# Kernel optimization log

Hardware: AMD Instinct MI355X
Metric: run time of the kernel (lower is better)

The kernel has to match this reference:

```python
import jax, jax.numpy as jnp
import numpy as np

BN_EPS = 1e-5


def _bn_relu(h, gamma, beta):
    # BatchNorm1d in training mode: normalize over (batch, length) per channel
    mean = h.mean(axis=(0, 2), keepdims=True)
    var = h.var(axis=(0, 2), keepdims=True)
    h = (h - mean) * jax.lax.rsqrt(var + BN_EPS)
    h = h * gamma[None, :, None] + beta[None, :, None]
    return jax.nn.relu(h)


def _gather(ldesc, idx):
    # ldesc: [B, D, N], idx: [B, M] -> [B, D, M]
    B, D, N = ldesc.shape
    M = idx.shape[1]
    return jnp.take_along_axis(ldesc, jnp.broadcast_to(idx[:, None, :], (B, D, M)), axis=2)


def _scatter_mean(src, idx, N):
    # per-batch scatter-mean: src [B, D, M], idx [B, M] -> [B, D, N]
    def one(s, i):
        D = s.shape[0]
        sums = jnp.zeros((D, N), s.dtype).at[:, i].add(s)
        cnts = jnp.zeros((N,), s.dtype).at[i].add(1.0)
        return sums / jnp.maximum(cnts, 1.0)[None, :]
    return jax.vmap(one)(src, idx)


def _endpoint_update(ldesc, line_enc, idx, W1, b1, g1, bt1, W2, b2):
    B, D, _ = ldesc.shape
    ld = _gather(ldesc, idx)                                   # [B, D, 2L]
    # flip endpoint pairs: neighbor endpoint of each endpoint
    neigh = ld.reshape(B, D, -1, 2)[..., ::-1].reshape(B, D, -1)
    msg = jnp.concatenate([ld, neigh, line_enc], axis=1)       # [B, 3D, 2L]
    h = jnp.einsum('oc,bcm->bom', W1, msg) + b1[None, :, None]  # Conv1d k=1
    h = _bn_relu(h, g1, bt1)
    out = jnp.einsum('oc,bcm->bom', W2, h) + b2[None, :, None]
    return out                                                  # [B, D, 2L]


def setup_inputs() -> dict:
    key = jax.random.key(0)
    ks = jax.random.split(key, 12)
    B, D, N, M = 8, 256, 8192, 8192
    inp = {
        'ldesc0': jax.random.normal(ks[0], (B, D, N), jnp.float32),
        'ldesc1': jax.random.normal(ks[1], (B, D, N), jnp.float32),
        'line_enc0': jax.random.normal(ks[2], (B, D, M), jnp.float32),
        'line_enc1': jax.random.normal(ks[3], (B, D, M), jnp.float32),
        'lines_junc_idx0': jax.random.randint(ks[4], (B, M), 0, N),
        'lines_junc_idx1': jax.random.randint(ks[5], (B, M), 0, N),
        'W1': jax.random.normal(ks[6], (2 * D, 3 * D), jnp.float32) * (1.0 / np.sqrt(3 * D)),
        'b1': jnp.zeros((2 * D,), jnp.float32),
        'g1': jnp.ones((2 * D,), jnp.float32),
        'bt1': jnp.zeros((2 * D,), jnp.float32),
        'W2': jax.random.normal(ks[7], (D, 2 * D), jnp.float32) * (1.0 / np.sqrt(2 * D)),
        'b2': jnp.zeros((D,), jnp.float32),
    }
    return inp


def reference(ldesc0, ldesc1, line_enc0, line_enc1, lines_junc_idx0, lines_junc_idx1,
              W1, b1, g1, bt1, W2, b2):
    N = ldesc0.shape[2]
    up0 = _endpoint_update(ldesc0, line_enc0, lines_junc_idx0, W1, b1, g1, bt1, W2, b2)
    up1 = _endpoint_update(ldesc1, line_enc1, lines_junc_idx1, W1, b1, g1, bt1, W2, b2)
    out0 = ldesc0 + _scatter_mean(up0, lines_junc_idx0, N)
    out1 = ldesc1 + _scatter_mean(up1, lines_junc_idx1, N)
    return (out0, out1)
```

## Files before the change

### kernel.cpp

```cpp
#include <hip/hip_runtime.h>
#include <hip/hip_bf16.h>

#define B_  8
#define D_  256
#define N_  8192
#define M_  8192
#define O1_ 512
#define K1_ 768
#define K2_ 512

typedef unsigned short u16;
typedef __attribute__((ext_vector_type(8))) short bf8;
typedef __attribute__((ext_vector_type(4))) float f4;

static __device__ __forceinline__ float bf2f(u16 u) {
    unsigned v = ((unsigned)u) << 16;
    return __uint_as_float(v);
}
static __device__ __forceinline__ u16 f2bf(float f) {
    __hip_bfloat16 h = __float2bfloat16(f);
    return *reinterpret_cast<u16*>(&h);
}
static __device__ __forceinline__ void gl_lds16(const u16* g, u16* l) {
    __builtin_amdgcn_global_load_lds((const __attribute__((address_space(1))) void*)g,
                                     (__attribute__((address_space(3))) void*)l, 16, 0, 0);
}
static __device__ __forceinline__ int swz64(int r) {
    return (((r >> 1) & 1) << 4) | (((r >> 2) & 1) << 5);
}

__global__ __launch_bounds__(256) void k_transpose_all(const float* __restrict__ s0, const float* __restrict__ s1,
                                                       const float* __restrict__ s2, const float* __restrict__ s3,
                                                       u16* __restrict__ dA, u16* __restrict__ dB) {
    __shared__ float t[32][33];
    const int z = blockIdx.z;
    const int sel = z >> 3, b = z & 7;
    const float* src = (sel == 0) ? s0 : (sel == 1) ? s1 : (sel == 2) ? s2 : s3;
    u16* dst = ((sel < 2) ? dA : dB) + (size_t)(sel & 1) * B_ * N_ * D_;
    const int c0 = blockIdx.x * 32, r0 = blockIdx.y * 32;
    const int tx = threadIdx.x, ty = threadIdx.y;
    const float* s = src + (size_t)b * D_ * N_;
    u16* d = dst + (size_t)b * N_ * D_;
#pragma unroll
    for (int i = 0; i < 4; ++i) {
        int r = r0 + ty + i * 8;
        t[ty + i * 8][tx] = s[(size_t)r * N_ + (c0 + tx)];
    }
    __syncthreads();
#pragma unroll
    for (int i = 0; i < 4; ++i) {
        int c = c0 + ty + i * 8;
        d[(size_t)c * D_ + (r0 + tx)] = f2bf(t[tx][ty + i * 8]);
    }
}

__global__ __launch_bounds__(256) void k_convert_w(const float* __restrict__ W1, const float* __restrict__ W2,
                                                   u16* __restrict__ W1b, u16* __restrict__ W2b) {
    int i = blockIdx.x * 256 + threadIdx.x;
    const int n1 = O1_ * K1_;
    const int n2 = D_ * K2_;
    if (i < n1) W1b[i] = f2bf(W1[i]);
    int j = i - n1;
    if (j >= 0 && j < n2) W2b[j] = f2bf(W2[j]);
}

#define NT1 12
__global__ __launch_bounds__(512, 2) void k_gemm1(const u16* __restrict__ W1b,
                                                  const u16* __restrict__ Tld2,
                                                  const u16* __restrict__ Tle2,
                                                  const int* __restrict__ idx0,
                                                  const int* __restrict__ idx1,
                                                  u16* __restrict__ hbuf2) {
    __shared__ u16 LA[2][2][256][32];
    __shared__ u16 LB[2][2][256][32];
    const int z  = blockIdx.z;
    const int side = z >> 3, b = z & 7;
    const u16* Tld = Tld2 + (size_t)side * B_ * N_ * D_;
    const u16* Tle = Tle2 + (size_t)side * B_ * N_ * D_;
    const int* idx = side ? idx1 : idx0;
    u16* hbuf = hbuf2 + (size_t)side * B_ * M_ * O1_;
    const int o0 = blockIdx.y * 256;
    const int m0 = blockIdx.x * 256;
    const int tid = threadIdx.x;
    const int w = tid >> 6, l = tid & 63;
    const int wr = w >> 2;
    const int wc = w & 3;

    const int srow   = tid >> 2;
    const int schunk = (tid & 3) * 16;

    int na[2], nb[2], mm[2];
    const u16* aS[2];
    int bcolu[2];
#pragma unroll
    for (int j = 0; j < 2; ++j) {
        int r = j * 128 + srow;
        int m = m0 + r;
        mm[j] = m;
        na[j] = idx[b * M_ + m];
        nb[j] = idx[b * M_ + (m ^ 1)];
        int swu = (schunk ^ swz64(r)) >> 1;
        aS[j]   = W1b + (size_t)(o0 + r) * K1_ + swu;
        bcolu[j] = swu;
    }

    int aOff[8], bOff[4];
#pragma unroll
    for (int i = 0; i < 8; ++i) {
        int r = wr * 128 + i * 16 + (l & 15);
        aOff[i] = r * 32 + ((((l >> 4) * 16) ^ swz64(r)) >> 1);
    }
#pragma unroll
    for (int j = 0; j < 4; ++j) {
        int r = wc * 64 + j * 16 + (l & 15);
        bOff[j] = r * 32 + ((((l >> 4) * 16) ^ swz64(r)) >> 1);
    }

#define STAGE_A1(kt, ks, buf)                                                        \
    {                                                                                \
        _Pragma("unroll")                                                            \
        for (int j = 0; j < 2; ++j)                                                  \
            gl_lds16(aS[j] + (kt) * 64 + (ks) * 32, &LA[buf][ks][j * 128][0] + tid * 8); \
    }
#define STAGE_B1(kt, ks, buf)                                                        \
    {                                                                                \
        const int seg = (kt) >> 2;                                                   \
        const int cb  = ((kt) & 3) * 64 + (ks) * 32;                                 \
        _Pragma("unroll")                                                            \
        for (int j = 0; j < 2; ++j) {                                                \
            const u16* s;                                                            \
            if (seg == 0)      s = Tld + (size_t)(b * N_ + na[j]) * D_ + cb + bcolu[j]; \
            else if (seg == 1) s = Tld + (size_t)(b * N_ + nb[j]) * D_ + cb + bcolu[j]; \
            else               s = Tle + (size_t)(b * M_ + mm[j]) * D_ + cb + bcolu[j]; \
            gl_lds16(s, &LB[buf][ks][j * 128][0] + tid * 8);                         \
        }                                                                            \
    }

    f4 acc[8][4];
#pragma unroll
    for (int i = 0; i < 8; ++i)
#pragma unroll
        for (int j = 0; j < 4; ++j) acc[i][j] = {0.f, 0.f, 0.f, 0.f};

    STAGE_A1(0, 0, 0); STAGE_B1(0, 0, 0);
    STAGE_A1(0, 1, 0); STAGE_B1(0, 1, 0);
    STAGE_A1(1, 0, 1); STAGE_B1(1, 0, 1);
    asm volatile("s_waitcnt vmcnt(8)" ::: "memory");
    __builtin_amdgcn_s_barrier();
    __builtin_amdgcn_sched_barrier(0);

    for (int t = 0; t < NT1; ++t) {
        const int bufp = t & 1, nbuf = bufp ^ 1;
        const u16* baseA0 = &LA[bufp][0][0][0];
        const u16* baseA1 = &LA[bufp][1][0][0];
        const u16* baseB0 = &LB[bufp][0][0][0];
        const u16* baseB1 = &LB[bufp][1][0][0];
        bf8 aF[4], bF[4];

#pragma unroll
        for (int j = 0; j < 4; ++j) bF[j] = *reinterpret_cast<const bf8*>(baseB0 + bOff[j]);
#pragma unroll
        for (int ii = 0; ii < 4; ++ii) aF[ii] = *reinterpret_cast<const bf8*>(baseA0 + aOff[ii]);
        if (t + 1 < NT1) STAGE_A1(t + 1, 1, nbuf);
        __builtin_amdgcn_s_barrier();
        asm volatile("s_waitcnt lgkmcnt(0)" ::: "memory");
        __builtin_amdgcn_sched_barrier(0);
        __builtin_amdgcn_s_setprio(1);
#pragma unroll
        for (int ii = 0; ii < 4; ++ii)
#pragma unroll
            for (int j = 0; j < 4; ++j)
                acc[ii][j] = __builtin_amdgcn_mfma_f32_16x16x32_bf16(aF[ii], bF[j], acc[ii][j], 0, 0, 0);
        __builtin_amdgcn_s_setprio(0);
        __builtin_amdgcn_s_barrier();
        __builtin_amdgcn_sched_barrier(0);

#pragma unroll
        for (int ii = 0; ii < 4; ++ii) aF[ii] = *reinterpret_cast<const bf8*>(baseA0 + aOff[4 + ii]);
        if (t + 1 < NT1) STAGE_B1(t + 1, 1, nbuf);
        __builtin_amdgcn_s_barrier();
        asm volatile("s_waitcnt lgkmcnt(0)" ::: "memory");
        __builtin_amdgcn_sched_barrier(0);
        __builtin_amdgcn_s_setprio(1);
#pragma unroll
        for (int ii = 0; ii < 4; ++ii)
#pragma unroll
            for (int j = 0; j < 4; ++j)
                acc[4 + ii][j] = __builtin_amdgcn_mfma_f32_16x16x32_bf16(aF[ii], bF[j], acc[4 + ii][j], 0, 0, 0);
        __builtin_amdgcn_s_setprio(0);
        if (t < NT1 - 2) asm volatile("s_waitcnt vmcnt(8)" ::: "memory");
        else             asm volatile("s_waitcnt vmcnt(0)" ::: "memory");
        __builtin_amdgcn_s_barrier();
        __builtin_amdgcn_sched_barrier(0);

#pragma unroll
        for (int j = 0; j < 4; ++j) bF[j] = *reinterpret_cast<const bf8*>(baseB1 + bOff[j]);
#pragma unroll
        for (int ii = 0; ii < 4; ++ii) aF[ii] = *reinterpret_cast<const bf8*>(baseA1 + aOff[ii]);
        if (t + 2 < NT1) STAGE_A1(t + 2, 0, bufp);
        __builtin_amdgcn_s_barrier();
        asm volatile("s_waitcnt lgkmcnt(0)" ::: "memory");
        __builtin_amdgcn_sched_barrier(0);
        __builtin_amdgcn_s_setprio(1);
#pragma unroll
        for (int ii = 0; ii < 4; ++ii)
#pragma unroll
            for (int j = 0; j < 4; ++j)
                acc[ii][j] = __builtin_amdgcn_mfma_f32_16x16x32_bf16(aF[ii], bF[j], acc[ii][j], 0, 0, 0);
        __builtin_amdgcn_s_setprio(0);
        __builtin_amdgcn_s_barrier();
        __builtin_amdgcn_sched_barrier(0);

#pragma unroll
        for (int ii = 0; ii < 4; ++ii) aF[ii] = *reinterpret_cast<const bf8*>(baseA1 + aOff[4 + ii]);
        if (t + 2 < NT1) STAGE_B1(t + 2, 0, bufp);
        __builtin_amdgcn_s_barrier();
        asm volatile("s_waitcnt lgkmcnt(0)" ::: "memory");
        __builtin_amdgcn_sched_barrier(0);
        __builtin_amdgcn_s_setprio(1);
#pragma unroll
        for (int ii = 0; ii < 4; ++ii)
#pragma unroll
            for (int j = 0; j < 4; ++j)
                acc[4 + ii][j] = __builtin_amdgcn_mfma_f32_16x16x32_bf16(aF[ii], bF[j], acc[4 + ii][j], 0, 0, 0);
        __builtin_amdgcn_s_setprio(0);
        if (t < NT1 - 2) asm volatile("s_waitcnt vmcnt(8)" ::: "memory");
        else             asm volatile("s_waitcnt vmcnt(0)" ::: "memory");
        __builtin_amdgcn_s_barrier();
        __builtin_amdgcn_sched_barrier(0);
    }
#undef STAGE_A1
#undef STAGE_B1

#pragma unroll
    for (int j = 0; j < 4; ++j) {
        int m = m0 + wc * 64 + j * 16 + (l & 15);
        size_t rowbase = (size_t)(b * M_ + m) * O1_;
#pragma unroll
        for (int i = 0; i < 8; ++i) {
            int orow = o0 + wr * 128 + i * 16 + (l >> 4) * 4;
            ushort4 pk;
            pk.x = f2bf(acc[i][j].x);
            pk.y = f2bf(acc[i][j].y);
            pk.z = f2bf(acc[i][j].z);
            pk.w = f2bf(acc[i][j].w);
            *reinterpret_cast<ushort4*>(&hbuf[rowbase + orow]) = pk;
        }
    }
}

__global__ __launch_bounds__(256) void k_stats(const u16* __restrict__ hbuf2, float* __restrict__ stats) {
    const int side = blockIdx.x >> 8;
    const int blk  = blockIdx.x & 255;
    const u16* hb = hbuf2 + (size_t)side * B_ * M_ * O1_;
    float* st = stats + side * 1024;
    const int t = threadIdx.x;
    const size_t row0 = (size_t)blk * 256;
    float s0 = 0.f, q0 = 0.f, s1 = 0.f, q1 = 0.f;
    for (int r = 0; r < 256; ++r) {
        const u16* p = hb + (row0 + r) * O1_;
        float v0 = bf2f(p[t]);
        float v1 = bf2f(p[t + 256]);
        s0 += v0; q0 += v0 * v0;
        s1 += v1; q1 += v1 * v1;
    }
    atomicAdd(&st[t], s0);
    atomicAdd(&st[O1_ + t], q0);
    atomicAdd(&st[t + 256], s1);
    atomicAdd(&st[O1_ + t + 256], q1);
}

__global__ void k_finalize_ac(const float* __restrict__ stats, const float* __restrict__ g1,
                              const float* __restrict__ bt1, float* __restrict__ ac) {
    int i = blockIdx.x * 256 + threadIdx.x;
    if (i >= 1024) return;
    int side = i >> 9, o = i & 511;
    const float* st = stats + side * 1024;
    const float inv = 1.0f / ((float)B_ * (float)M_);
    float mean = st[o] * inv;
    float var  = st[O1_ + o] * inv - mean * mean;
    var = fmaxf(var, 0.0f);
    float a = g1[o] * rsqrtf(var + 1e-5f);
    ac[side * 1024 + o] = a;
    ac[side * 1024 + O1_ + o] = bt1[o] - mean * a;
}

__global__ void k_count_int(const int* __restrict__ idx0, const int* __restrict__ idx1, int* __restrict__ cnt2) {
    int i = blockIdx.x * 256 + threadIdx.x;
    if (i < 2 * B_ * M_) {
        int side = i >> 16, j = i & 65535;
        const int* idx = side ? idx1 : idx0;
        atomicAdd(&cnt2[side * B_ * N_ + (j >> 13) * N_ + idx[j]], 1);
    }
}

__global__ __launch_bounds__(1024) void k_scan(const int* __restrict__ cnt2, int* __restrict__ offs2,
                                               int* __restrict__ fill2) {
    __shared__ int wsum[1024];
    const int base = blockIdx.x * N_;
    const int t = threadIdx.x;
    int v[8]; int s = 0;
#pragma unroll
    for (int k = 0; k < 8; ++k) { v[k] = cnt2[base + t * 8 + k]; s += v[k]; }
    wsum[t] = s;
    __syncthreads();
    for (int off = 1; off < 1024; off <<= 1) {
        int add = (t >= off) ? wsum[t - off] : 0;
        __syncthreads();
        wsum[t] += add;
        __syncthreads();
    }
    int run = (t > 0) ? wsum[t - 1] : 0;
#pragma unroll
    for (int k = 0; k < 8; ++k) {
        offs2[base + t * 8 + k] = run;
        fill2[base + t * 8 + k] = run;
        run += v[k];
    }
}

__global__ void k_fill(const int* __restrict__ idx0, const int* __restrict__ idx1,
                       int* __restrict__ fill2, int* __restrict__ mlist2) {
    int i = blockIdx.x * 256 + threadIdx.x;
    if (i < 2 * B_ * M_) {
        int side = i >> 16, j = i & 65535;
        const int* idx = side ? idx1 : idx0;
        int b = j >> 13, m = j & (M_ - 1);
        int pos = atomicAdd(&fill2[side * B_ * N_ + b * N_ + idx[j]], 1);
        mlist2[(size_t)side * B_ * M_ + b * M_ + pos] = m;
    }
}

__global__ __launch_bounds__(256) void k_gemm2(const u16* __restrict__ W2b,
                                               const u16* __restrict__ hbuf2,
                                               const float* __restrict__ ac,
                                               const float* __restrict__ b2,
                                               u16* __restrict__ up2) {
    __shared__ u16 At[128 * 32];
    __shared__ u16 Bt[128 * 32];
    __shared__ float acs[1024];
    const int z = blockIdx.z;
    const int side = z >> 3, b = z & 7;
    const u16* hbuf = hbuf2 + (size_t)side * B_ * M_ * O1_;
    u16* up = up2 + (size_t)side * B_ * M_ * D_;
    const float* acp = ac + side * 1024;
    const int d0 = blockIdx.y * 128;
    const int m0 = blockIdx.x * 128;
    const int tid = threadIdx.x;
    const int w = tid >> 6, l = tid & 63;
    const int lr = l >> 2, lc = (l & 3) * 8;

    acs[tid]       = acp[tid];
    acs[tid + 256] = acp[tid + 256];
    acs[tid + 512] = acp[tid + 512];
    acs[tid + 768] = acp[tid + 768];

    const u16* pA[2]; const u16* pB[2];
#pragma unroll
    for (int t = 0; t < 2; ++t) {
        int row = t * 64 + w * 16 + lr;
        pA[t] = W2b + (size_t)(d0 + row) * K2_ + lc;
        int m  = m0 + row;
        pB[t] = hbuf + (size_t)(b * M_ + m) * O1_ + lc;
    }
    const int wr = w >> 1, wc = w & 1;
    f4 acc[4][4];
#pragma unroll
    for (int i = 0; i < 4; ++i)
#pragma unroll
        for (int j = 0; j < 4; ++j) acc[i][j] = {0.f, 0.f, 0.f, 0.f};

    const int aoff = (wr * 64 + (l & 15)) * 32 + (l >> 4) * 8;
    const int boff = (wc * 64 + (l & 15)) * 32 + (l >> 4) * 8;
    const int bdst = (w * 16 + lr) * 32 + lc;

    __syncthreads();

    for (int kk = 0; kk < 16; ++kk) {
        const int o = kk * 32 + lc;
        f4 A0 = *reinterpret_cast<const f4*>(&acs[o]);
        f4 A1 = *reinterpret_cast<const f4*>(&acs[o + 4]);
        f4 C0 = *reinterpret_cast<const f4*>(&acs[512 + o]);
        f4 C1 = *reinterpret_cast<const f4*>(&acs[512 + o + 4]);
#pragma unroll
        for (int t = 0; t < 2; ++t) {
            gl_lds16(pA[t] + kk * 32, At + (t * 64 + w * 16) * 32);
            const ushort4* ps = reinterpret_cast<const ushort4*>(pB[t] + kk * 32);
            ushort4 v0 = ps[0], v1 = ps[1];
            union { ushort4 u4[2]; bf8 v8; } pk;
            pk.u4[0].x = f2bf(fmaxf(bf2f(v0.x) * A0.x + C0.x, 0.0f));
            pk.u4[0].y = f2bf(fmaxf(bf2f(v0.y) * A0.y + C0.y, 0.0f));
            pk.u4[0].z = f2bf(fmaxf(bf2f(v0.z) * A0.z + C0.z, 0.0f));
            pk.u4[0].w = f2bf(fmaxf(bf2f(v0.w) * A0.w + C0.w, 0.0f));
            pk.u4[1].x = f2bf(fmaxf(bf2f(v1.x) * A1.x + C1.x, 0.0f));
            pk.u4[1].y = f2bf(fmaxf(bf2f(v1.y) * A1.y + C1.y, 0.0f));
            pk.u4[1].z = f2bf(fmaxf(bf2f(v1.z) * A1.z + C1.z, 0.0f));
            pk.u4[1].w = f2bf(fmaxf(bf2f(v1.w) * A1.w + C1.w, 0.0f));
            *reinterpret_cast<bf8*>(&Bt[t * 64 * 32 + bdst]) = pk.v8;
        }
        __syncthreads();
        bf8 aF[4], bF[4];
#pragma unroll
        for (int i = 0; i < 4; ++i) aF[i] = *reinterpret_cast<const bf8*>(&At[aoff + i * 16 * 32]);
#pragma unroll
        for (int j = 0; j < 4; ++j) bF[j] = *reinterpret_cast<const bf8*>(&Bt[boff + j * 16 * 32]);
#pragma unroll
        for (int i = 0; i < 4; ++i)
#pragma unroll
            for (int j = 0; j < 4; ++j)
                acc[i][j] = __builtin_amdgcn_mfma_f32_16x16x32_bf16(aF[i], bF[j], acc[i][j], 0, 0, 0);
        __syncthreads();
    }

#pragma unroll
    for (int j = 0; j < 4; ++j) {
        int m = m0 + wc * 64 + j * 16 + (l & 15);
        size_t rowbase = (size_t)(b * M_ + m) * D_;
#pragma unroll
        for (int i = 0; i < 4; ++i) {
            int d = d0 + wr * 64 + i * 16 + (l >> 4) * 4;
            ushort4 pk;
            pk.x = f2bf(acc[i][j].x + b2[d + 0]);
            pk.y = f2bf(acc[i][j].y + b2[d + 1]);
            pk.z = f2bf(acc[i][j].z + b2[d + 2]);
            pk.w = f2bf(acc[i][j].w + b2[d + 3]);
            *reinterpret_cast<ushort4*>(&up[rowbase + d]) = pk;
        }
    }
}

__global__ __launch_bounds__(256) void k_reduce_finalize(const float* __restrict__ ldesc0,
                                                         const float* __restrict__ ldesc1,
                                                         const u16* __restrict__ up2,
                                                         const int* __restrict__ cnt2,
                                                         const int* __restrict__ offs2,
                                                         const int* __restrict__ mlist2,
                                                         float* __restrict__ out) {
    __shared__ float lds[32][257];
    const int z = blockIdx.z;
    const int side = z >> 3, b = z & 7;
    const float* ldesc = side ? ldesc1 : ldesc0;
    const u16* up = up2 + (size_t)side * B_ * M_ * D_;
    const int* cnt  = cnt2  + side * B_ * N_;
    const int* offs = offs2 + side * B_ * N_;
    const int* mlist = mlist2 + (size_t)side * B_ * M_;
    float* outp = out + (size_t)side * B_ * D_ * N_;
    const int n0 = blockIdx.x * 32;
    const int tx = threadIdx.x, ty = threadIdx.y;
#pragma unroll
    for (int i = 0; i < 4; ++i) {
        int nl = ty + i * 8;
        int n  = n0 + nl;
        int c   = cnt[b * N_ + n];
        int off = offs[b * N_ + n];
        float inv = 1.0f / (float)max(c, 1);
        float acc[8] = {0.f, 0.f, 0.f, 0.f, 0.f, 0.f, 0.f, 0.f};
        for (int e = 0; e < c; ++e) {
            int m = mlist[(size_t)b * M_ + off + e];
            const ushort4* row = reinterpret_cast<const ushort4*>(up + (size_t)(b * M_ + m) * D_ + tx * 8);
            ushort4 aa = row[0], bb = row[1];
            acc[0] += bf2f(aa.x); acc[1] += bf2f(aa.y); acc[2] += bf2f(aa.z); acc[3] += bf2f(aa.w);
            acc[4] += bf2f(bb.x); acc[5] += bf2f(bb.y); acc[6] += bf2f(bb.z); acc[7] += bf2f(bb.w);
        }
#pragma unroll
        for (int k = 0; k < 8; ++k) lds[nl][tx * 8 + k] = acc[k] * inv;
    }
    __syncthreads();
#pragma unroll
    for (int i = 0; i < 32; ++i) {
        int d = ty + i * 8;
        size_t o2 = (size_t)(b * D_ + d) * N_ + n0 + tx;
        outp[o2] = ldesc[o2] + lds[tx][d];
    }
}

__global__ void k_marker(float* out, float v) { out[0] = v; }

extern "C" void kernel_launch(void* const* d_in, const int* in_sizes, int n_in,
                              void* d_out, int out_size, void* d_ws, size_t ws_size,
                              hipStream_t stream) {
    const float* ldesc0 = (const float*)d_in[0];
    const float* ldesc1 = (const float*)d_in[1];
    const float* le0    = (const float*)d_in[2];
    const float* le1    = (const float*)d_in[3];
    const int*   idx0   = (const int*)d_in[4];
    const int*   idx1   = (const int*)d_in[5];
    const float* W1     = (const float*)d_in[6];
    const float* g1     = (const float*)d_in[8];
    const float* bt1    = (const float*)d_in[9];
    const float* W2     = (const float*)d_in[10];
    const float* b2     = (const float*)d_in[11];
    float* out = (float*)d_out;

    char* ws = (char*)d_ws;
    const size_t SIDE_BND = (size_t)B_ * N_ * D_ * 2;
    const size_t oTld2  = 0;
    const size_t oTle2  = 2 * SIDE_BND;
    const size_t oH2    = 4 * SIDE_BND;
    const size_t oW1b   = oH2 + (size_t)2 * B_ * M_ * O1_ * 2;
    const size_t oW2b   = oW1b + 786432;
    const size_t oStats = oW2b + 262144;
    const size_t oAC    = oStats + 8192;
    const size_t NEED   = oAC + 8192;
    if (ws_size < NEED) {
        k_marker<<<1, 1, 0, stream>>>(out, 1000.0f + (float)(ws_size >> 20));
        return;
    }
    u16*   Tld2  = (u16*)(ws + oTld2);
    u16*   up2   = (u16*)(ws + oTld2);
    u16*   Tle2  = (u16*)(ws + oTle2);
    int*   cnt2  = (int*)(ws + oTle2);
    int*   offs2 = (int*)(ws + oTle2 + 524288);
    int*   fill2 = (int*)(ws + oTle2 + 1048576);
    int*   mlist2= (int*)(ws + oTle2 + 1572864);
    u16*   hbuf2 = (u16*)(ws + oH2);
    u16*   W1b   = (u16*)(ws + oW1b);
    u16*   W2b   = (u16*)(ws + oW2b);
    float* stats = (float*)(ws + oStats);
    float* ac    = (float*)(ws + oAC);

    k_convert_w<<<2048, 256, 0, stream>>>(W1, W2, W1b, W2b);

    const dim3 tb(32, 8);
    k_transpose_all<<<dim3(N_ / 32, D_ / 32, 32), tb, 0, stream>>>(ldesc0, ldesc1, le0, le1, Tld2, Tle2);
    k_gemm1<<<dim3(M_ / 256, O1_ / 256, 16), 512, 0, stream>>>(W1b, Tld2, Tle2, idx0, idx1, hbuf2);
    hipMemsetAsync(stats, 0, 8192, stream);
    k_stats<<<512, 256, 0, stream>>>(hbuf2, stats);
    k_finalize_ac<<<4, 256, 0, stream>>>(stats, g1, bt1, ac);
    hipMemsetAsync(cnt2, 0, (size_t)2 * B_ * N_ * 4, stream);
    k_count_int<<<2 * B_ * M_ / 256, 256, 0, stream>>>(idx0, idx1, cnt2);
    k_scan<<<16, 1024, 0, stream>>>(cnt2, offs2, fill2);
    k_fill<<<2 * B_ * M_ / 256, 256, 0, stream>>>(idx0, idx1, fill2, mlist2);
    k_gemm2<<<dim3(M_ / 128, D_ / 128, 16), 256, 0, stream>>>(W2b, hbuf2, ac, b2, up2);
    k_reduce_finalize<<<dim3(N_ / 32, 1, 16), tb, 0, stream>>>(ldesc0, ldesc1, up2, cnt2, offs2, mlist2, out);
}
```

Baseline: 412.9 us.

## Fuse BN statistics into GEMM1 epilogue and retile GEMM2 to full output width

Per-channel sum and sum-of-squares are now computed from the GEMM1 accumulators with shuffle and LDS reductions plus atomics, which removes the separate k_stats kernel that re-read the whole bf16 hidden buffer. Because the statistics now come from fp32 accumulators rather than bf16-rounded values, they differ slightly from before. GEMM2 is retiled to 512 threads covering all 256 output channels per block, so the BN+ReLU transform of each hidden tile is computed once instead of twice. GEMM2 also gains XOR-swizzled LDS layouts and a bias array cached in LDS.

```diff
diff --git a/kernel.cpp b/kernel.cpp
--- a/kernel.cpp
+++ b/kernel.cpp
@@ -70,7 +70,8 @@
                                                   const u16* __restrict__ Tle2,
                                                   const int* __restrict__ idx0,
                                                   const int* __restrict__ idx1,
-                                                  u16* __restrict__ hbuf2) {
+                                                  u16* __restrict__ hbuf2,
+                                                  float* __restrict__ stats) {
     __shared__ u16 LA[2][2][256][32];
     __shared__ u16 LB[2][2][256][32];
     const int z  = blockIdx.z;
@@ -232,6 +233,35 @@
 #undef STAGE_A1
 #undef STAGE_B1
 
+    float* redS = (float*)&LA[0][0][0][0];
+    float* redQ = (float*)&LA[0][0][0][0] + 1024;
+#pragma unroll
+    for (int i = 0; i < 8; ++i) {
+#pragma unroll
+        for (int r = 0; r < 4; ++r) {
+            float s = acc[i][0][r] + acc[i][1][r] + acc[i][2][r] + acc[i][3][r];
+            float q = acc[i][0][r] * acc[i][0][r] + acc[i][1][r] * acc[i][1][r]
+                    + acc[i][2][r] * acc[i][2][r] + acc[i][3][r] * acc[i][3][r];
+#pragma unroll
+            for (int mk = 1; mk < 16; mk <<= 1) {
+                s += __shfl_xor(s, mk, 16);
+                q += __shfl_xor(q, mk, 16);
+            }
+            if ((l & 15) == 0) {
+                int ch = wr * 128 + i * 16 + (l >> 4) * 4 + r;
+                redS[ch * 4 + wc] = s;
+                redQ[ch * 4 + wc] = q;
+            }
+        }
+    }
+    __syncthreads();
+    if (tid < 256) {
+        float s = redS[tid * 4] + redS[tid * 4 + 1] + redS[tid * 4 + 2] + redS[tid * 4 + 3];
+        float q = redQ[tid * 4] + redQ[tid * 4 + 1] + redQ[tid * 4 + 2] + redQ[tid * 4 + 3];
+        atomicAdd(&stats[side * 1024 + o0 + tid], s);
+        atomicAdd(&stats[side * 1024 + 512 + o0 + tid], q);
+    }
+
 #pragma unroll
     for (int j = 0; j < 4; ++j) {
         int m = m0 + wc * 64 + j * 16 + (l & 15);
@@ -247,27 +277,6 @@
             *reinterpret_cast<ushort4*>(&hbuf[rowbase + orow]) = pk;
         }
     }
-}
-
-__global__ __launch_bounds__(256) void k_stats(const u16* __restrict__ hbuf2, float* __restrict__ stats) {
-    const int side = blockIdx.x >> 8;
-    const int blk  = blockIdx.x & 255;
-    const u16* hb = hbuf2 + (size_t)side * B_ * M_ * O1_;
-    float* st = stats + side * 1024;
-    const int t = threadIdx.x;
-    const size_t row0 = (size_t)blk * 256;
-    float s0 = 0.f, q0 = 0.f, s1 = 0.f, q1 = 0.f;
-    for (int r = 0; r < 256; ++r) {
-        const u16* p = hb + (row0 + r) * O1_;
-        float v0 = bf2f(p[t]);
-        float v1 = bf2f(p[t + 256]);
-        s0 += v0; q0 += v0 * v0;
-        s1 += v1; q1 += v1 * v1;
-    }
-    atomicAdd(&st[t], s0);
-    atomicAdd(&st[O1_ + t], q0);
-    atomicAdd(&st[t + 256], s1);
-    atomicAdd(&st[O1_ + t + 256], q1);
 }
 
 __global__ void k_finalize_ac(const float* __restrict__ stats, const float* __restrict__ g1,
@@ -331,61 +340,74 @@
     }
 }
 
-__global__ __launch_bounds__(256) void k_gemm2(const u16* __restrict__ W2b,
+__global__ __launch_bounds__(512) void k_gemm2(const u16* __restrict__ W2b,
                                                const u16* __restrict__ hbuf2,
                                                const float* __restrict__ ac,
                                                const float* __restrict__ b2,
                                                u16* __restrict__ up2) {
-    __shared__ u16 At[128 * 32];
+    __shared__ u16 At[256 * 32];
     __shared__ u16 Bt[128 * 32];
     __shared__ float acs[1024];
+    __shared__ float bcs[256];
     const int z = blockIdx.z;
     const int side = z >> 3, b = z & 7;
     const u16* hbuf = hbuf2 + (size_t)side * B_ * M_ * O1_;
     u16* up = up2 + (size_t)side * B_ * M_ * D_;
     const float* acp = ac + side * 1024;
-    const int d0 = blockIdx.y * 128;
     const int m0 = blockIdx.x * 128;
     const int tid = threadIdx.x;
     const int w = tid >> 6, l = tid & 63;
-    const int lr = l >> 2, lc = (l & 3) * 8;
+    const int wr = w >> 2;
+    const int wc = w & 3;
 
     acs[tid]       = acp[tid];
-    acs[tid + 256] = acp[tid + 256];
     acs[tid + 512] = acp[tid + 512];
-    acs[tid + 768] = acp[tid + 768];
-
-    const u16* pA[2]; const u16* pB[2];
-#pragma unroll
-    for (int t = 0; t < 2; ++t) {
-        int row = t * 64 + w * 16 + lr;
-        pA[t] = W2b + (size_t)(d0 + row) * K2_ + lc;
-        int m  = m0 + row;
-        pB[t] = hbuf + (size_t)(b * M_ + m) * O1_ + lc;
-    }
-    const int wr = w >> 1, wc = w & 1;
-    f4 acc[4][4];
-#pragma unroll
-    for (int i = 0; i < 4; ++i)
-#pragma unroll
-        for (int j = 0; j < 4; ++j) acc[i][j] = {0.f, 0.f, 0.f, 0.f};
-
-    const int aoff = (wr * 64 + (l & 15)) * 32 + (l >> 4) * 8;
-    const int boff = (wc * 64 + (l & 15)) * 32 + (l >> 4) * 8;
-    const int bdst = (w * 16 + lr) * 32 + lc;
+    if (tid < 256) bcs[tid] = b2[tid];
+
+    const int srow   = tid >> 2;
+    const int schunk = (tid & 3) * 16;
+    const int lcu    = (tid & 3) * 8;
+
+    const u16* aS[2];
+#pragma unroll
+    for (int j = 0; j < 2; ++j) {
+        int r = j * 128 + srow;
+        aS[j] = W2b + (size_t)r * K2_ + ((schunk ^ swz64(r)) >> 1);
+    }
+    const u16* pB = hbuf + (size_t)(b * M_ + m0 + srow) * O1_ + lcu;
+    u16* bDst = &Bt[srow * 32 + ((schunk ^ swz64(srow)) >> 1)];
+
+    int aOff[8], bOff[2];
+#pragma unroll
+    for (int i = 0; i < 8; ++i) {
+        int r = wr * 128 + i * 16 + (l & 15);
+        aOff[i] = r * 32 + ((((l >> 4) * 16) ^ swz64(r)) >> 1);
+    }
+#pragma unroll
+    for (int j = 0; j < 2; ++j) {
+        int r = wc * 32 + j * 16 + (l & 15);
+        bOff[j] = r * 32 + ((((l >> 4) * 16) ^ swz64(r)) >> 1);
+    }
+
+    f4 acc[8][2];
+#pragma unroll
+    for (int i = 0; i < 8; ++i)
+#pragma unroll
+        for (int j = 0; j < 2; ++j) acc[i][j] = {0.f, 0.f, 0.f, 0.f};
 
     __syncthreads();
 
     for (int kk = 0; kk < 16; ++kk) {
-        const int o = kk * 32 + lc;
+        const int o = kk * 32 + lcu;
         f4 A0 = *reinterpret_cast<const f4*>(&acs[o]);
         f4 A1 = *reinterpret_cast<const f4*>(&acs[o + 4]);
         f4 C0 = *reinterpret_cast<const f4*>(&acs[512 + o]);
         f4 C1 = *reinterpret_cast<const f4*>(&acs[512 + o + 4]);
 #pragma unroll
-        for (int t = 0; t < 2; ++t) {
-            gl_lds16(pA[t] + kk * 32, At + (t * 64 + w * 16) * 32);
-            const ushort4* ps = reinterpret_cast<const ushort4*>(pB[t] + kk * 32);
+        for (int j = 0; j < 2; ++j)
+            gl_lds16(aS[j] + kk * 32, At + j * 128 * 32 + tid * 8);
+        {
+            const ushort4* ps = reinterpret_cast<const ushort4*>(pB + kk * 32);
             ushort4 v0 = ps[0], v1 = ps[1];
             union { ushort4 u4[2]; bf8 v8; } pk;
             pk.u4[0].x = f2bf(fmaxf(bf2f(v0.x) * A0.x + C0.x, 0.0f));
@@ -396,34 +418,34 @@
             pk.u4[1].y = f2bf(fmaxf(bf2f(v1.y) * A1.y + C1.y, 0.0f));
             pk.u4[1].z = f2bf(fmaxf(bf2f(v1.z) * A1.z + C1.z, 0.0f));
             pk.u4[1].w = f2bf(fmaxf(bf2f(v1.w) * A1.w + C1.w, 0.0f));
-            *reinterpret_cast<bf8*>(&Bt[t * 64 * 32 + bdst]) = pk.v8;
+            *reinterpret_cast<bf8*>(bDst) = pk.v8;
         }
         __syncthreads();
-        bf8 aF[4], bF[4];
-#pragma unroll
-        for (int i = 0; i < 4; ++i) aF[i] = *reinterpret_cast<const bf8*>(&At[aoff + i * 16 * 32]);
-#pragma unroll
-        for (int j = 0; j < 4; ++j) bF[j] = *reinterpret_cast<const bf8*>(&Bt[boff + j * 16 * 32]);
-#pragma unroll
-        for (int i = 0; i < 4; ++i)
-#pragma unroll
-            for (int j = 0; j < 4; ++j)
+        bf8 aF[8], bF[2];
+#pragma unroll
+        for (int i = 0; i < 8; ++i) aF[i] = *reinterpret_cast<const bf8*>(&At[aOff[i]]);
+#pragma unroll
+        for (int j = 0; j < 2; ++j) bF[j] = *reinterpret_cast<const bf8*>(&Bt[bOff[j]]);
+#pragma unroll
+        for (int i = 0; i < 8; ++i)
+#pragma unroll
+            for (int j = 0; j < 2; ++j)
                 acc[i][j] = __builtin_amdgcn_mfma_f32_16x16x32_bf16(aF[i], bF[j], acc[i][j], 0, 0, 0);
         __syncthreads();
     }
 
 #pragma unroll
-    for (int j = 0; j < 4; ++j) {
-        int m = m0 + wc * 64 + j * 16 + (l & 15);
+    for (int j = 0; j < 2; ++j) {
+        int m = m0 + wc * 32 + j * 16 + (l & 15);
         size_t rowbase = (size_t)(b * M_ + m) * D_;
 #pragma unroll
-        for (int i = 0; i < 4; ++i) {
-            int d = d0 + wr * 64 + i * 16 + (l >> 4) * 4;
+        for (int i = 0; i < 8; ++i) {
+            int d = wr * 128 + i * 16 + (l >> 4) * 4;
             ushort4 pk;
-            pk.x = f2bf(acc[i][j].x + b2[d + 0]);
-            pk.y = f2bf(acc[i][j].y + b2[d + 1]);
-            pk.z = f2bf(acc[i][j].z + b2[d + 2]);
-            pk.w = f2bf(acc[i][j].w + b2[d + 3]);
+            pk.x = f2bf(acc[i][j].x + bcs[d + 0]);
+            pk.y = f2bf(acc[i][j].y + bcs[d + 1]);
+            pk.z = f2bf(acc[i][j].z + bcs[d + 2]);
+            pk.w = f2bf(acc[i][j].w + bcs[d + 3]);
             *reinterpret_cast<ushort4*>(&up[rowbase + d]) = pk;
         }
     }
@@ -523,14 +545,13 @@
 
     const dim3 tb(32, 8);
     k_transpose_all<<<dim3(N_ / 32, D_ / 32, 32), tb, 0, stream>>>(ldesc0, ldesc1, le0, le1, Tld2, Tle2);
-    k_gemm1<<<dim3(M_ / 256, O1_ / 256, 16), 512, 0, stream>>>(W1b, Tld2, Tle2, idx0, idx1, hbuf2);
     hipMemsetAsync(stats, 0, 8192, stream);
-    k_stats<<<512, 256, 0, stream>>>(hbuf2, stats);
+    k_gemm1<<<dim3(M_ / 256, O1_ / 256, 16), 512, 0, stream>>>(W1b, Tld2, Tle2, idx0, idx1, hbuf2, stats);
     k_finalize_ac<<<4, 256, 0, stream>>>(stats, g1, bt1, ac);
     hipMemsetAsync(cnt2, 0, (size_t)2 * B_ * N_ * 4, stream);
     k_count_int<<<2 * B_ * M_ / 256, 256, 0, stream>>>(idx0, idx1, cnt2);
     k_scan<<<16, 1024, 0, stream>>>(cnt2, offs2, fill2);
     k_fill<<<2 * B_ * M_ / 256, 256, 0, stream>>>(idx0, idx1, fill2, mlist2);
-    k_gemm2<<<dim3(M_ / 128, D_ / 128, 16), 256, 0, stream>>>(W2b, hbuf2, ac, b2, up2);
+    k_gemm2<<<dim3(M_ / 128, 1, 16), 512, 0, stream>>>(W2b, hbuf2, ac, b2, up2);
     k_reduce_finalize<<<dim3(N_ / 32, 1, 16), tb, 0, stream>>>(ldesc0, ldesc1, up2, cnt2, offs2, mlist2, out);
 }
```

Result: no change. 413.6 us (+0.2%).
